# Optimization experiments

Measured on AMD Instinct MI355X. Metric: run time of the kernel, lower is better.

Reference implementation:

```python
import jax, jax.numpy as jnp
import numpy as np


def setup_inputs() -> dict:
    key = jax.random.key(0)
    kq, kk = jax.random.split(key)
    B, Q, K, D = 32, 512, 512, 1024
    queries = jax.random.normal(kq, (B, Q, D), dtype=jnp.float32)
    keys = jax.random.normal(kk, (B, K, D), dtype=jnp.float32)
    # ProbabilityConverter learned scalars (is_temperature=True, is_bias=True)
    temperature = jnp.ones((), dtype=jnp.float32)
    bias = jnp.zeros((), dtype=jnp.float32)
    return {"queries": queries, "keys": keys, "temperature": temperature, "bias": bias}


def reference(queries, keys, temperature, bias):
    # Dot scoring: (B, Q, D) x (B, K, D) -> (B, Q, K)
    logits = jnp.einsum("bqd,bkd->bqk", queries, keys)
    # keys.eq(0.0)[:, :, :1].transpose(1, 2): mask positions where first key feature == 0
    key_mask = (keys[:, :, 0] == 0.0)[:, None, :]  # (B, 1, K)
    neg_inf = jnp.array(-jnp.inf, dtype=logits.dtype)
    logits = jnp.where(key_mask, neg_inf, logits)
    # confidence = sigmoid((logsumexp(logits) + bias) * temperature)
    approx_max_logit = jax.nn.logsumexp(logits, axis=-1)  # (B, Q)
    confidence = jax.nn.sigmoid((approx_max_logit + bias) * temperature)
    attn = jax.nn.softmax(logits, axis=-1)  # (B, Q, K)
    return attn, confidence
```

## Files before the change

kernel.cpp:

```cpp
#include <hip/hip_runtime.h>
#include <math.h>
#include <stdint.h>


#define NB 32
#define NQ 512
#define NK 512
#define ND 1024
#define BK 32
#define NT (ND / BK)
#define BM1 64
#define BM2 32
#define TILE_BYTES 65536
#define WS_TILES ((size_t)NB * NT * TILE_BYTES)
#define WS_TOTAL (WS_TILES + (size_t)NB * NK * 4)

typedef __attribute__((ext_vector_type(8))) short short8;
typedef __attribute__((ext_vector_type(4))) float f32x4;

__device__ __forceinline__ void bf_split(float x, unsigned& hbits, float& lo) {
  unsigned u = __float_as_uint(x);
  unsigned r = u + 0x7fffu + ((u >> 16) & 1u);
  hbits = r & 0xffff0000u;
  lo = x - __uint_as_float(hbits);
}
__device__ __forceinline__ unsigned pack_rn(float x0, float x1) {
  unsigned u0 = __float_as_uint(x0), u1 = __float_as_uint(x1);
  unsigned r0 = u0 + 0x7fffu + ((u0 >> 16) & 1u);
  unsigned r1 = u1 + 0x7fffu + ((u1 >> 16) & 1u);
  return (r0 >> 16) | (r1 & 0xffff0000u);
}

__device__ __forceinline__ int lds_off_write(int r, int c4) {
  int slot = ((c4 >> 1) + (r >> 1)) & 3;
  return r * 32 + slot * 8 + (c4 & 1) * 4;
}
__device__ __forceinline__ int lds_off_read(int r, int quad) {
  int slot = (quad + (r >> 1)) & 3;
  return r * 32 + slot * 8;
}

__device__ __forceinline__ void gl2lds16(const void* g, void* l) {
  __builtin_amdgcn_global_load_lds(
      (const __attribute__((address_space(1))) unsigned int*)g,
      (__attribute__((address_space(3))) unsigned int*)l, 16, 0, 0);
}

__global__ __launch_bounds__(256)
void convert_k(const float* __restrict__ Kg, unsigned char* __restrict__ ws) {
  const int bx = blockIdx.x;
  const int batch = bx >> 5, kt = bx & 31;
  const float* src = Kg + (size_t)batch * NK * ND + kt * BK;
  unsigned short* hiB = (unsigned short*)(ws + (size_t)bx * TILE_BYTES);
  unsigned short* loB = hiB + 32768 / 2;
  float* maskB = (float*)(ws + WS_TILES) + batch * NK;

#pragma unroll
  for (int i = 0; i < 16; ++i) {
    int idx = threadIdx.x + 256 * i;
    int r = idx >> 3, c4 = idx & 7;
    float4 v = *(const float4*)(src + (size_t)r * ND + c4 * 4);
    unsigned h0, h1, h2, h3;
    float l0, l1, l2, l3;
    bf_split(v.x, h0, l0); bf_split(v.y, h1, l1);
    bf_split(v.z, h2, l2); bf_split(v.w, h3, l3);
    int off = lds_off_write(r, c4);
    *(uint2*)(&hiB[off]) = make_uint2((h0 >> 16) | h1, (h2 >> 16) | h3);
    *(uint2*)(&loB[off]) = make_uint2(pack_rn(l0, l1), pack_rn(l2, l3));
    if (kt == 0 && c4 == 0) maskB[r] = v.x;
  }
}

__global__ __launch_bounds__(256, 2)
void attn_fused_v2(const float* __restrict__ Qg,
                   const unsigned char* __restrict__ ws,
                   const float* __restrict__ Tp, const float* __restrict__ Bp,
                   float* __restrict__ attn, float* __restrict__ conf) {
  __shared__ __align__(16) unsigned short sBhi[NK * BK];
  __shared__ __align__(16) unsigned short sBlo[NK * BK];
  __shared__ __align__(16) unsigned short sAhi[BM2 * BK];
  __shared__ __align__(16) unsigned short sAlo[BM2 * BK];
  __shared__ float sRedA[4][BM2];
  __shared__ float sRedB[4][BM2];

  const int tid = threadIdx.x;
  const int g = blockIdx.x;
  const int batch = (g & 7) | (((g >> 3) & 3) << 3);
  const int q0 = (g >> 5) * BM2;
  const int ln = tid & 63, w = tid >> 6;
  const int ln15 = ln & 15, quad = ln >> 4;
  const int wn0 = w * 128;

  const float* Qp = Qg + ((size_t)batch * NQ + q0) * ND;
  const unsigned char* wsB = ws + (size_t)batch * NT * TILE_BYTES;
  const float* maskB = (const float*)(ws + WS_TILES) + batch * NK;

  f32x4 acc[2][8];
#pragma unroll
  for (int mt = 0; mt < 2; ++mt)
#pragma unroll
    for (int nt = 0; nt < 8; ++nt) acc[mt][nt] = (f32x4){0.f, 0.f, 0.f, 0.f};

  const int ar = tid >> 3, ac4 = tid & 7;
  float4 pa = *(const float4*)(Qp + (size_t)ar * ND + ac4 * 4);

  for (int kt = 0; kt < NT; ++kt) {
    if (kt) __syncthreads();

    const unsigned char* tb = wsB + (size_t)kt * TILE_BYTES;
#pragma unroll
    for (int c = 0; c < 8; ++c) {
      int byte = (((c * 4 + w) * 64) + ln) * 16;
      gl2lds16(tb + byte, ((unsigned char*)sBhi) + byte);
      gl2lds16(tb + 32768 + byte, ((unsigned char*)sBlo) + byte);
    }
    {
      unsigned h0, h1, h2, h3;
      float l0, l1, l2, l3;
      bf_split(pa.x, h0, l0); bf_split(pa.y, h1, l1);
      bf_split(pa.z, h2, l2); bf_split(pa.w, h3, l3);
      int off = lds_off_write(ar, ac4);
      *(uint2*)(&sAhi[off]) = make_uint2((h0 >> 16) | h1, (h2 >> 16) | h3);
      *(uint2*)(&sAlo[off]) = make_uint2(pack_rn(l0, l1), pack_rn(l2, l3));
    }
    __syncthreads();

    if (kt + 1 < NT)
      pa = *(const float4*)(Qp + (kt + 1) * BK + (size_t)ar * ND + ac4 * 4);

    short8 ahi[2], alo[2];
#pragma unroll
    for (int mt = 0; mt < 2; ++mt) {
      int off = lds_off_read(mt * 16 + ln15, quad);
      ahi[mt] = *(const short8*)(&sAhi[off]);
      alo[mt] = *(const short8*)(&sAlo[off]);
    }
#pragma unroll
    for (int nt = 0; nt < 8; ++nt) {
      int off = lds_off_read(wn0 + nt * 16 + ln15, quad);
      short8 bhi = *(const short8*)(&sBhi[off]);
      short8 blo = *(const short8*)(&sBlo[off]);
#pragma unroll
      for (int mt = 0; mt < 2; ++mt) {
        acc[mt][nt] = __builtin_amdgcn_mfma_f32_16x16x32_bf16(ahi[mt], bhi, acc[mt][nt], 0, 0, 0);
        acc[mt][nt] = __builtin_amdgcn_mfma_f32_16x16x32_bf16(ahi[mt], blo, acc[mt][nt], 0, 0, 0);
        acc[mt][nt] = __builtin_amdgcn_mfma_f32_16x16x32_bf16(alo[mt], bhi, acc[mt][nt], 0, 0, 0);
      }
    }
  }

  const float NEGINF = -__builtin_inff();
  float rm[2][4];
#pragma unroll
  for (int mt = 0; mt < 2; ++mt)
#pragma unroll
    for (int rg = 0; rg < 4; ++rg) rm[mt][rg] = NEGINF;

#pragma unroll
  for (int nt = 0; nt < 8; ++nt) {
    int col = wn0 + nt * 16 + ln15;
    bool msk = (maskB[col] == 0.0f);
#pragma unroll
    for (int mt = 0; mt < 2; ++mt)
#pragma unroll
      for (int rg = 0; rg < 4; ++rg) {
        float v = msk ? NEGINF : acc[mt][nt][rg];
        acc[mt][nt][rg] = v;
        rm[mt][rg] = fmaxf(rm[mt][rg], v);
      }
  }
#pragma unroll
  for (int mt = 0; mt < 2; ++mt)
#pragma unroll
    for (int rg = 0; rg < 4; ++rg) {
      float v = rm[mt][rg];
#pragma unroll
      for (int d = 1; d < 16; d <<= 1) v = fmaxf(v, __shfl_xor(v, d, 64));
      rm[mt][rg] = v;
    }
  if (ln15 == 0) {
#pragma unroll
    for (int mt = 0; mt < 2; ++mt)
#pragma unroll
      for (int rg = 0; rg < 4; ++rg)
        sRedA[w][mt * 16 + quad * 4 + rg] = rm[mt][rg];
  }
  __syncthreads();

  float gmax[2][4], gsum[2][4];
#pragma unroll
  for (int mt = 0; mt < 2; ++mt)
#pragma unroll
    for (int rg = 0; rg < 4; ++rg) {
      int row = mt * 16 + quad * 4 + rg;
      gmax[mt][rg] = fmaxf(fmaxf(sRedA[0][row], sRedA[1][row]),
                           fmaxf(sRedA[2][row], sRedA[3][row]));
      gsum[mt][rg] = 0.f;
    }

#pragma unroll
  for (int nt = 0; nt < 8; ++nt)
#pragma unroll
    for (int mt = 0; mt < 2; ++mt)
#pragma unroll
      for (int rg = 0; rg < 4; ++rg) {
        float e = __expf(acc[mt][nt][rg] - gmax[mt][rg]);
        acc[mt][nt][rg] = e;
        gsum[mt][rg] += e;
      }
#pragma unroll
  for (int mt = 0; mt < 2; ++mt)
#pragma unroll
    for (int rg = 0; rg < 4; ++rg) {
      float v = gsum[mt][rg];
#pragma unroll
      for (int d = 1; d < 16; d <<= 1) v += __shfl_xor(v, d, 64);
      gsum[mt][rg] = v;
    }
  if (ln15 == 0) {
#pragma unroll
    for (int mt = 0; mt < 2; ++mt)
#pragma unroll
      for (int rg = 0; rg < 4; ++rg)
        sRedB[w][mt * 16 + quad * 4 + rg] = gsum[mt][rg];
  }
  __syncthreads();
#pragma unroll
  for (int mt = 0; mt < 2; ++mt)
#pragma unroll
    for (int rg = 0; rg < 4; ++rg) {
      int row = mt * 16 + quad * 4 + rg;
      gsum[mt][rg] = sRedB[0][row] + sRedB[1][row] + sRedB[2][row] + sRedB[3][row];
    }

  float* outBase = attn + ((size_t)batch * NQ + q0) * NK;
#pragma unroll
  for (int mt = 0; mt < 2; ++mt)
#pragma unroll
    for (int rg = 0; rg < 4; ++rg) {
      int row = mt * 16 + quad * 4 + rg;
      float inv = 1.0f / gsum[mt][rg];
#pragma unroll
      for (int nt = 0; nt < 8; ++nt)
        outBase[(size_t)row * NK + wn0 + nt * 16 + ln15] = acc[mt][nt][rg] * inv;
    }

  if (w == 0 && ln15 == 0) {
    float tv = Tp[0], bv = Bp[0];
#pragma unroll
    for (int mt = 0; mt < 2; ++mt)
#pragma unroll
      for (int rg = 0; rg < 4; ++rg) {
        int row = mt * 16 + quad * 4 + rg;
        float lse = gmax[mt][rg] + __logf(gsum[mt][rg]);
        float t = (lse + bv) * tv;
        conf[(size_t)batch * NQ + q0 + row] = 1.0f / (1.0f + __expf(-t));
      }
  }
}

__global__ __launch_bounds__(256, 1)
void attn_fused_v1(const float* __restrict__ Qg, const float* __restrict__ Kg,
                   const float* __restrict__ Tp, const float* __restrict__ Bp,
                   float* __restrict__ attn, float* __restrict__ conf) {
  __shared__ __align__(16) unsigned short sAhi[BM1 * BK];
  __shared__ __align__(16) unsigned short sAlo[BM1 * BK];
  __shared__ __align__(16) unsigned short sBhi[NK * BK];
  __shared__ __align__(16) unsigned short sBlo[NK * BK];
  __shared__ float sRedA[4][BM1];
  __shared__ float sRedB[4][BM1];

  const int tid = threadIdx.x;
  const int g = blockIdx.x;
  const int batch = (g & 7) | (((g >> 3) & 3) << 3);
  const int q0 = (g >> 5) * BM1;
  const int ln = tid & 63, w = tid >> 6;
  const int ln15 = ln & 15, quad = ln >> 4;
  const int wn0 = w * 128;

  const float* Qp = Qg + ((size_t)batch * NQ + q0) * ND;
  const float* Kp = Kg + (size_t)batch * NK * ND;

  f32x4 acc[4][8];
#pragma unroll
  for (int mt = 0; mt < 4; ++mt)
#pragma unroll
    for (int nt = 0; nt < 8; ++nt) acc[mt][nt] = (f32x4){0.f, 0.f, 0.f, 0.f};

  float4 pb[16], pa[2];
#pragma unroll
  for (int i = 0; i < 16; ++i) {
    int idx = tid + 256 * i, r = idx >> 3, c4 = idx & 7;
    pb[i] = *(const float4*)(Kp + (size_t)r * ND + c4 * 4);
  }
#pragma unroll
  for (int i = 0; i < 2; ++i) {
    int idx = tid + 256 * i, r = idx >> 3, c4 = idx & 7;
    pa[i] = *(const float4*)(Qp + (size_t)r * ND + c4 * 4);
  }

  for (int kt = 0; kt < NT; ++kt) {
    if (kt) __syncthreads();
#pragma unroll
    for (int i = 0; i < 2; ++i) {
      int idx = tid + 256 * i, r = idx >> 3, c4 = idx & 7;
      int off = lds_off_write(r, c4);
      unsigned h0, h1, h2, h3; float l0, l1, l2, l3;
      bf_split(pa[i].x, h0, l0); bf_split(pa[i].y, h1, l1);
      bf_split(pa[i].z, h2, l2); bf_split(pa[i].w, h3, l3);
      *(uint2*)(&sAhi[off]) = make_uint2((h0 >> 16) | h1, (h2 >> 16) | h3);
      *(uint2*)(&sAlo[off]) = make_uint2(pack_rn(l0, l1), pack_rn(l2, l3));
    }
#pragma unroll
    for (int i = 0; i < 16; ++i) {
      int idx = tid + 256 * i, r = idx >> 3, c4 = idx & 7;
      int off = lds_off_write(r, c4);
      unsigned h0, h1, h2, h3; float l0, l1, l2, l3;
      bf_split(pb[i].x, h0, l0); bf_split(pb[i].y, h1, l1);
      bf_split(pb[i].z, h2, l2); bf_split(pb[i].w, h3, l3);
      *(uint2*)(&sBhi[off]) = make_uint2((h0 >> 16) | h1, (h2 >> 16) | h3);
      *(uint2*)(&sBlo[off]) = make_uint2(pack_rn(l0, l1), pack_rn(l2, l3));
    }
    __syncthreads();

    if (kt < NT - 1) {
      const float* Kq = Kp + (kt + 1) * BK;
      const float* Qq = Qp + (kt + 1) * BK;
#pragma unroll
      for (int i = 0; i < 16; ++i) {
        int idx = tid + 256 * i, r = idx >> 3, c4 = idx & 7;
        pb[i] = *(const float4*)(Kq + (size_t)r * ND + c4 * 4);
      }
#pragma unroll
      for (int i = 0; i < 2; ++i) {
        int idx = tid + 256 * i, r = idx >> 3, c4 = idx & 7;
        pa[i] = *(const float4*)(Qq + (size_t)r * ND + c4 * 4);
      }
    }

    short8 ahi[4], alo[4];
#pragma unroll
    for (int mt = 0; mt < 4; ++mt) {
      int off = lds_off_read(mt * 16 + ln15, quad);
      ahi[mt] = *(const short8*)(&sAhi[off]);
      alo[mt] = *(const short8*)(&sAlo[off]);
    }
#pragma unroll
    for (int nt = 0; nt < 8; ++nt) {
      int off = lds_off_read(wn0 + nt * 16 + ln15, quad);
      short8 bhi = *(const short8*)(&sBhi[off]);
      short8 blo = *(const short8*)(&sBlo[off]);
#pragma unroll
      for (int mt = 0; mt < 4; ++mt) {
        acc[mt][nt] = __builtin_amdgcn_mfma_f32_16x16x32_bf16(ahi[mt], bhi, acc[mt][nt], 0, 0, 0);
        acc[mt][nt] = __builtin_amdgcn_mfma_f32_16x16x32_bf16(ahi[mt], blo, acc[mt][nt], 0, 0, 0);
        acc[mt][nt] = __builtin_amdgcn_mfma_f32_16x16x32_bf16(alo[mt], bhi, acc[mt][nt], 0, 0, 0);
      }
    }
  }

  const float NEGINF = -__builtin_inff();
  float rm[4][4];
#pragma unroll
  for (int mt = 0; mt < 4; ++mt)
#pragma unroll
    for (int rg = 0; rg < 4; ++rg) rm[mt][rg] = NEGINF;
#pragma unroll
  for (int nt = 0; nt < 8; ++nt) {
    int col = wn0 + nt * 16 + ln15;
    bool msk = (Kp[(size_t)col * ND] == 0.0f);
#pragma unroll
    for (int mt = 0; mt < 4; ++mt)
#pragma unroll
      for (int rg = 0; rg < 4; ++rg) {
        float v = msk ? NEGINF : acc[mt][nt][rg];
        acc[mt][nt][rg] = v;
        rm[mt][rg] = fmaxf(rm[mt][rg], v);
      }
  }
#pragma unroll
  for (int mt = 0; mt < 4; ++mt)
#pragma unroll
    for (int rg = 0; rg < 4; ++rg) {
      float v = rm[mt][rg];
#pragma unroll
      for (int d = 1; d < 16; d <<= 1) v = fmaxf(v, __shfl_xor(v, d, 64));
      rm[mt][rg] = v;
    }
  if (ln15 == 0)
#pragma unroll
    for (int mt = 0; mt < 4; ++mt)
#pragma unroll
      for (int rg = 0; rg < 4; ++rg)
        sRedA[w][mt * 16 + quad * 4 + rg] = rm[mt][rg];
  __syncthreads();

  float gmax[4][4], gsum[4][4];
#pragma unroll
  for (int mt = 0; mt < 4; ++mt)
#pragma unroll
    for (int rg = 0; rg < 4; ++rg) {
      int row = mt * 16 + quad * 4 + rg;
      gmax[mt][rg] = fmaxf(fmaxf(sRedA[0][row], sRedA[1][row]),
                           fmaxf(sRedA[2][row], sRedA[3][row]));
      gsum[mt][rg] = 0.f;
    }
#pragma unroll
  for (int nt = 0; nt < 8; ++nt)
#pragma unroll
    for (int mt = 0; mt < 4; ++mt)
#pragma unroll
      for (int rg = 0; rg < 4; ++rg) {
        float e = __expf(acc[mt][nt][rg] - gmax[mt][rg]);
        acc[mt][nt][rg] = e;
        gsum[mt][rg] += e;
      }
#pragma unroll
  for (int mt = 0; mt < 4; ++mt)
#pragma unroll
    for (int rg = 0; rg < 4; ++rg) {
      float v = gsum[mt][rg];
#pragma unroll
      for (int d = 1; d < 16; d <<= 1) v += __shfl_xor(v, d, 64);
      gsum[mt][rg] = v;
    }
  if (ln15 == 0)
#pragma unroll
    for (int mt = 0; mt < 4; ++mt)
#pragma unroll
      for (int rg = 0; rg < 4; ++rg)
        sRedB[w][mt * 16 + quad * 4 + rg] = gsum[mt][rg];
  __syncthreads();
#pragma unroll
  for (int mt = 0; mt < 4; ++mt)
#pragma unroll
    for (int rg = 0; rg < 4; ++rg) {
      int row = mt * 16 + quad * 4 + rg;
      gsum[mt][rg] = sRedB[0][row] + sRedB[1][row] + sRedB[2][row] + sRedB[3][row];
    }

  float* outBase = attn + ((size_t)batch * NQ + q0) * NK;
#pragma unroll
  for (int mt = 0; mt < 4; ++mt)
#pragma unroll
    for (int rg = 0; rg < 4; ++rg) {
      int row = mt * 16 + quad * 4 + rg;
      float inv = 1.0f / gsum[mt][rg];
#pragma unroll
      for (int nt = 0; nt < 8; ++nt)
        outBase[(size_t)row * NK + wn0 + nt * 16 + ln15] = acc[mt][nt][rg] * inv;
    }
  if (w == 0 && ln15 == 0) {
    float tv = Tp[0], bv = Bp[0];
#pragma unroll
    for (int mt = 0; mt < 4; ++mt)
#pragma unroll
      for (int rg = 0; rg < 4; ++rg) {
        int row = mt * 16 + quad * 4 + rg;
        float lse = gmax[mt][rg] + __logf(gsum[mt][rg]);
        float t = (lse + bv) * tv;
        conf[(size_t)batch * NQ + q0 + row] = 1.0f / (1.0f + __expf(-t));
      }
  }
}

extern "C" void kernel_launch(void* const* d_in, const int* in_sizes, int n_in,
                              void* d_out, int out_size, void* d_ws, size_t ws_size,
                              hipStream_t stream) {
  const float* q = (const float*)d_in[0];
  const float* k = (const float*)d_in[1];
  const float* temp = (const float*)d_in[2];
  const float* bias = (const float*)d_in[3];
  float* attn = (float*)d_out;
  float* conf = attn + (size_t)NB * NQ * NK;

  if (ws_size >= WS_TOTAL) {
    hipLaunchKernelGGL(convert_k, dim3(NB * NT), dim3(256), 0, stream,
                       k, (unsigned char*)d_ws);
    hipLaunchKernelGGL(attn_fused_v2, dim3(NB * (NQ / BM2)), dim3(256), 0, stream,
                       q, (const unsigned char*)d_ws, temp, bias, attn, conf);
  } else {
    hipLaunchKernelGGL(attn_fused_v1, dim3(NB * (NQ / BM1)), dim3(256), 0, stream,
                       q, k, temp, bias, attn, conf);
  }
}
```

Before: 226.9 us.

## Double-buffer LDS tiles in a 1024-thread, 64-row fused attention kernel

Replaces the 256-thread, 32-row-per-block kernel with a 1024-thread block covering 64 query rows and 16 waves (2x8 wave grid). K and Q tiles are double-buffered in LDS, so the next tile is prefetched while MFMAs run on the current one, leaving one barrier per k-step. Each staged K tile now serves twice as many query rows, which halves K traffic per output. In exchange, LDS use roughly doubles to about 136 KB per block, the cross-wave max and sum reductions span 8 column waves, and occupancy drops to one large block per CU.

```diff
diff --git a/kernel.cpp b/kernel.cpp
--- a/kernel.cpp
+++ b/kernel.cpp
@@ -10,7 +10,7 @@
 #define BK 32
 #define NT (ND / BK)
 #define BM1 64
-#define BM2 32
+#define BM3 64
 #define TILE_BYTES 65536
 #define WS_TILES ((size_t)NB * NT * TILE_BYTES)
 #define WS_TOTAL (WS_TILES + (size_t)NB * NK * 4)
@@ -71,75 +71,95 @@
   }
 }
 
-__global__ __launch_bounds__(256, 2)
-void attn_fused_v2(const float* __restrict__ Qg,
+__device__ __forceinline__ void stage_a(unsigned short* hiA, unsigned short* loA,
+                                        int ar, int ac4, float4 v) {
+  unsigned h0, h1, h2, h3;
+  float l0, l1, l2, l3;
+  bf_split(v.x, h0, l0); bf_split(v.y, h1, l1);
+  bf_split(v.z, h2, l2); bf_split(v.w, h3, l3);
+  int off = lds_off_write(ar, ac4);
+  *(uint2*)(&hiA[off]) = make_uint2((h0 >> 16) | h1, (h2 >> 16) | h3);
+  *(uint2*)(&loA[off]) = make_uint2(pack_rn(l0, l1), pack_rn(l2, l3));
+}
+
+__device__ __forceinline__ void stage_b(const unsigned char* tb,
+                                        unsigned short* hiB, unsigned short* loB,
+                                        int w, int ln) {
+  int b0 = (w * 64 + ln) * 16;
+  int b1 = ((16 + w) * 64 + ln) * 16;
+  gl2lds16(tb + b0, ((unsigned char*)hiB) + b0);
+  gl2lds16(tb + b1, ((unsigned char*)hiB) + b1);
+  gl2lds16(tb + 32768 + b0, ((unsigned char*)loB) + b0);
+  gl2lds16(tb + 32768 + b1, ((unsigned char*)loB) + b1);
+}
+
+__global__ __launch_bounds__(1024, 4)
+void attn_fused_v3(const float* __restrict__ Qg,
                    const unsigned char* __restrict__ ws,
                    const float* __restrict__ Tp, const float* __restrict__ Bp,
                    float* __restrict__ attn, float* __restrict__ conf) {
-  __shared__ __align__(16) unsigned short sBhi[NK * BK];
-  __shared__ __align__(16) unsigned short sBlo[NK * BK];
-  __shared__ __align__(16) unsigned short sAhi[BM2 * BK];
-  __shared__ __align__(16) unsigned short sAlo[BM2 * BK];
-  __shared__ float sRedA[4][BM2];
-  __shared__ float sRedB[4][BM2];
+  __shared__ __align__(16) unsigned short sBhi[2][NK * BK];
+  __shared__ __align__(16) unsigned short sBlo[2][NK * BK];
+  __shared__ __align__(16) unsigned short sAhi[2][BM3 * BK];
+  __shared__ __align__(16) unsigned short sAlo[2][BM3 * BK];
+  __shared__ float sRedA[8][BM3];
+  __shared__ float sRedB[8][BM3];
 
   const int tid = threadIdx.x;
   const int g = blockIdx.x;
   const int batch = (g & 7) | (((g >> 3) & 3) << 3);
-  const int q0 = (g >> 5) * BM2;
+  const int q0 = (g >> 5) * BM3;
   const int ln = tid & 63, w = tid >> 6;
   const int ln15 = ln & 15, quad = ln >> 4;
-  const int wn0 = w * 128;
+  const int wc = w & 7, wr = w >> 3;
+  const int row0 = wr * 32, col0 = wc * 64;
 
   const float* Qp = Qg + ((size_t)batch * NQ + q0) * ND;
   const unsigned char* wsB = ws + (size_t)batch * NT * TILE_BYTES;
   const float* maskB = (const float*)(ws + WS_TILES) + batch * NK;
 
-  f32x4 acc[2][8];
-#pragma unroll
-  for (int mt = 0; mt < 2; ++mt)
-#pragma unroll
-    for (int nt = 0; nt < 8; ++nt) acc[mt][nt] = (f32x4){0.f, 0.f, 0.f, 0.f};
-
+  f32x4 acc[2][4];
+#pragma unroll
+  for (int mt = 0; mt < 2; ++mt)
+#pragma unroll
+    for (int nt = 0; nt < 4; ++nt) acc[mt][nt] = (f32x4){0.f, 0.f, 0.f, 0.f};
+
+  const bool aload = (tid < 512);
   const int ar = tid >> 3, ac4 = tid & 7;
-  float4 pa = *(const float4*)(Qp + (size_t)ar * ND + ac4 * 4);
+
+  float4 pa = (float4){0.f, 0.f, 0.f, 0.f};
+  if (aload) {
+    float4 a0 = *(const float4*)(Qp + (size_t)ar * ND + ac4 * 4);
+    stage_a(sAhi[0], sAlo[0], ar, ac4, a0);
+    pa = *(const float4*)(Qp + BK + (size_t)ar * ND + ac4 * 4);
+  }
+  stage_b(wsB, sBhi[0], sBlo[0], w, ln);
 
   for (int kt = 0; kt < NT; ++kt) {
-    if (kt) __syncthreads();
-
-    const unsigned char* tb = wsB + (size_t)kt * TILE_BYTES;
-#pragma unroll
-    for (int c = 0; c < 8; ++c) {
-      int byte = (((c * 4 + w) * 64) + ln) * 16;
-      gl2lds16(tb + byte, ((unsigned char*)sBhi) + byte);
-      gl2lds16(tb + 32768 + byte, ((unsigned char*)sBlo) + byte);
-    }
-    {
-      unsigned h0, h1, h2, h3;
-      float l0, l1, l2, l3;
-      bf_split(pa.x, h0, l0); bf_split(pa.y, h1, l1);
-      bf_split(pa.z, h2, l2); bf_split(pa.w, h3, l3);
-      int off = lds_off_write(ar, ac4);
-      *(uint2*)(&sAhi[off]) = make_uint2((h0 >> 16) | h1, (h2 >> 16) | h3);
-      *(uint2*)(&sAlo[off]) = make_uint2(pack_rn(l0, l1), pack_rn(l2, l3));
-    }
+    const int cur = kt & 1, nxt = cur ^ 1;
     __syncthreads();
 
-    if (kt + 1 < NT)
-      pa = *(const float4*)(Qp + (kt + 1) * BK + (size_t)ar * ND + ac4 * 4);
+    if (kt + 1 < NT) {
+      stage_b(wsB + (size_t)(kt + 1) * TILE_BYTES, sBhi[nxt], sBlo[nxt], w, ln);
+      if (aload) {
+        stage_a(sAhi[nxt], sAlo[nxt], ar, ac4, pa);
+        if (kt + 2 < NT)
+          pa = *(const float4*)(Qp + (kt + 2) * BK + (size_t)ar * ND + ac4 * 4);
+      }
+    }
 
     short8 ahi[2], alo[2];
 #pragma unroll
     for (int mt = 0; mt < 2; ++mt) {
-      int off = lds_off_read(mt * 16 + ln15, quad);
-      ahi[mt] = *(const short8*)(&sAhi[off]);
-      alo[mt] = *(const short8*)(&sAlo[off]);
-    }
-#pragma unroll
-    for (int nt = 0; nt < 8; ++nt) {
-      int off = lds_off_read(wn0 + nt * 16 + ln15, quad);
-      short8 bhi = *(const short8*)(&sBhi[off]);
-      short8 blo = *(const short8*)(&sBlo[off]);
+      int off = lds_off_read(row0 + mt * 16 + ln15, quad);
+      ahi[mt] = *(const short8*)(&sAhi[cur][off]);
+      alo[mt] = *(const short8*)(&sAlo[cur][off]);
+    }
+#pragma unroll
+    for (int nt = 0; nt < 4; ++nt) {
+      int off = lds_off_read(col0 + nt * 16 + ln15, quad);
+      short8 bhi = *(const short8*)(&sBhi[cur][off]);
+      short8 blo = *(const short8*)(&sBlo[cur][off]);
 #pragma unroll
       for (int mt = 0; mt < 2; ++mt) {
         acc[mt][nt] = __builtin_amdgcn_mfma_f32_16x16x32_bf16(ahi[mt], bhi, acc[mt][nt], 0, 0, 0);
@@ -157,8 +177,8 @@
     for (int rg = 0; rg < 4; ++rg) rm[mt][rg] = NEGINF;
 
 #pragma unroll
-  for (int nt = 0; nt < 8; ++nt) {
-    int col = wn0 + nt * 16 + ln15;
+  for (int nt = 0; nt < 4; ++nt) {
+    int col = col0 + nt * 16 + ln15;
     bool msk = (maskB[col] == 0.0f);
 #pragma unroll
     for (int mt = 0; mt < 2; ++mt)
@@ -178,12 +198,13 @@
       for (int d = 1; d < 16; d <<= 1) v = fmaxf(v, __shfl_xor(v, d, 64));
       rm[mt][rg] = v;
     }
+  __syncthreads();
   if (ln15 == 0) {
 #pragma unroll
     for (int mt = 0; mt < 2; ++mt)
 #pragma unroll
       for (int rg = 0; rg < 4; ++rg)
-        sRedA[w][mt * 16 + quad * 4 + rg] = rm[mt][rg];
+        sRedA[wc][row0 + mt * 16 + quad * 4 + rg] = rm[mt][rg];
   }
   __syncthreads();
 
@@ -192,14 +213,16 @@
   for (int mt = 0; mt < 2; ++mt)
 #pragma unroll
     for (int rg = 0; rg < 4; ++rg) {
-      int row = mt * 16 + quad * 4 + rg;
-      gmax[mt][rg] = fmaxf(fmaxf(sRedA[0][row], sRedA[1][row]),
-                           fmaxf(sRedA[2][row], sRedA[3][row]));
+      int row = row0 + mt * 16 + quad * 4 + rg;
+      float m = sRedA[0][row];
+#pragma unroll
+      for (int c = 1; c < 8; ++c) m = fmaxf(m, sRedA[c][row]);
+      gmax[mt][rg] = m;
       gsum[mt][rg] = 0.f;
     }
 
 #pragma unroll
-  for (int nt = 0; nt < 8; ++nt)
+  for (int nt = 0; nt < 4; ++nt)
 #pragma unroll
     for (int mt = 0; mt < 2; ++mt)
 #pragma unroll
@@ -222,15 +245,18 @@
     for (int mt = 0; mt < 2; ++mt)
 #pragma unroll
       for (int rg = 0; rg < 4; ++rg)
-        sRedB[w][mt * 16 + quad * 4 + rg] = gsum[mt][rg];
+        sRedB[wc][row0 + mt * 16 + quad * 4 + rg] = gsum[mt][rg];
   }
   __syncthreads();
 #pragma unroll
   for (int mt = 0; mt < 2; ++mt)
 #pragma unroll
     for (int rg = 0; rg < 4; ++rg) {
-      int row = mt * 16 + quad * 4 + rg;
-      gsum[mt][rg] = sRedB[0][row] + sRedB[1][row] + sRedB[2][row] + sRedB[3][row];
+      int row = row0 + mt * 16 + quad * 4 + rg;
+      float s = sRedB[0][row];
+#pragma unroll
+      for (int c = 1; c < 8; ++c) s += sRedB[c][row];
+      gsum[mt][rg] = s;
     }
 
   float* outBase = attn + ((size_t)batch * NQ + q0) * NK;
@@ -238,20 +264,20 @@
   for (int mt = 0; mt < 2; ++mt)
 #pragma unroll
     for (int rg = 0; rg < 4; ++rg) {
-      int row = mt * 16 + quad * 4 + rg;
+      int row = row0 + mt * 16 + quad * 4 + rg;
       float inv = 1.0f / gsum[mt][rg];
 #pragma unroll
-      for (int nt = 0; nt < 8; ++nt)
-        outBase[(size_t)row * NK + wn0 + nt * 16 + ln15] = acc[mt][nt][rg] * inv;
-    }
-
-  if (w == 0 && ln15 == 0) {
+      for (int nt = 0; nt < 4; ++nt)
+        outBase[(size_t)row * NK + col0 + nt * 16 + ln15] = acc[mt][nt][rg] * inv;
+    }
+
+  if (wc == 0 && ln15 == 0) {
     float tv = Tp[0], bv = Bp[0];
 #pragma unroll
     for (int mt = 0; mt < 2; ++mt)
 #pragma unroll
       for (int rg = 0; rg < 4; ++rg) {
-        int row = mt * 16 + quad * 4 + rg;
+        int row = row0 + mt * 16 + quad * 4 + rg;
         float lse = gmax[mt][rg] + __logf(gsum[mt][rg]);
         float t = (lse + bv) * tv;
         conf[(size_t)batch * NQ + q0 + row] = 1.0f / (1.0f + __expf(-t));
@@ -477,7 +503,7 @@
   if (ws_size >= WS_TOTAL) {
     hipLaunchKernelGGL(convert_k, dim3(NB * NT), dim3(256), 0, stream,
                        k, (unsigned char*)d_ws);
-    hipLaunchKernelGGL(attn_fused_v2, dim3(NB * (NQ / BM2)), dim3(256), 0, stream,
+    hipLaunchKernelGGL(attn_fused_v3, dim3(NB * (NQ / BM3)), dim3(1024), 0, stream,
                        q, (const unsigned char*)d_ws, temp, bias, attn, conf);
   } else {
     hipLaunchKernelGGL(attn_fused_v1, dim3(NB * (NQ / BM1)), dim3(256), 0, stream,
```

Result: faster. 219.6 us (-3.2%).
